# Performance work log

Measured on AMD Instinct MI355X. Metric: run time of the kernel, lower is better.

## Reference

```python
import jax, jax.numpy as jnp
import numpy as np

B, T_DEC, T_ENC = 64, 2048, 512
G_STEPS = 20000          # guided_att_steps
GAMMA = 0.99995          # guided_att_gamma


def setup_inputs() -> dict:
    key = jax.random.key(0)
    k1, k2, k3 = jax.random.split(key, 3)
    alignments = jax.random.uniform(k1, (B, T_DEC, T_ENC), dtype=jnp.float32)
    # ragged lengths in [dim/2, dim] (avoid zero-length -> div by zero)
    input_lengths = jax.random.randint(k2, (B,), T_ENC // 2, T_ENC + 1, dtype=jnp.int32)
    target_lengths = jax.random.randint(k3, (B,), T_DEC // 2, T_DEC + 1, dtype=jnp.int32)
    return {
        "alignments": alignments,
        "input_lengths": input_lengths,
        "target_lengths": target_lengths,
        "global_step": 10000,
    }


def reference(alignments, input_lengths, target_lengths, global_step):
    # matches torch: if self._g_steps < global_step: return 0
    if G_STEPS < global_step:
        return jnp.zeros((), dtype=alignments.dtype)
    g = GAMMA ** global_step  # python float constant
    inv_denom = 1.0 / (2.0 * g * g)

    F = target_lengths.astype(jnp.float32)[:, None, None]   # [B,1,1]
    L = input_lengths.astype(jnp.float32)[:, None, None]    # [B,1,1]
    f = jnp.arange(T_DEC, dtype=jnp.float32)[None, :, None]  # [1,T_dec,1]
    l = jnp.arange(T_ENC, dtype=jnp.float32)[None, None, :]  # [1,1,T_enc]

    # ragged diagonal gaussian mask, zero outside valid [f<F, l<L] region
    w = 1.0 - jnp.exp(-((l / L - f / F) ** 2) * inv_denom)   # [B,T_dec,T_enc]
    valid = (f < F) & (l < L)
    w = jnp.where(valid, w, 0.0)

    per_sample = jnp.sum(w * alignments, axis=(1, 2))        # [B]
    loss = jnp.mean(per_sample / target_lengths.astype(jnp.float32))
    return loss
```

## Files before the change

kernel.cpp:

```cpp
#include <hip/hip_runtime.h>
#include <math.h>


#define BB     64
#define TDEC   2048
#define TENC   512
#define GSTEPS 20000
#define GAMMA  0.99995

#define CHUNKS_PER_B (TDEC * (TENC / 4))
#define TOTAL_CHUNKS (BB * CHUNKS_PER_B)

__global__ void gal_prologue(const int* __restrict__ step_p,
                             float* __restrict__ ws,
                             float* __restrict__ out) {
    int step = step_p[0];
    double g = pow((double)GAMMA, (double)step);
    double inv_denom = 1.0 / (2.0 * g * g);
    ws[0] = (float)inv_denom;
    ((int*)ws)[1] = (GSTEPS < step) ? 0 : 1;
    out[0] = 0.0f;
}

__global__ __launch_bounds__(256) void gal_main(
    const float* __restrict__ align,
    const int* __restrict__ in_len,
    const int* __restrict__ tgt_len,
    const float* __restrict__ ws,
    float* __restrict__ out) {

    const float inv_denom = ws[0];
    const int active = ((const int*)ws)[1];
    if (!active) return;

    __shared__ int   sF[BB];
    __shared__ int   sL[BB];
    __shared__ float sInvF[BB];
    __shared__ float sInvL[BB];
    __shared__ float sScale[BB];
    if (threadIdx.x < BB) {
        int b = threadIdx.x;
        int F = tgt_len[b];
        int L = in_len[b];
        sF[b] = F;
        sL[b] = L;
        float invF = 1.0f / (float)F;
        sInvF[b] = invF;
        sInvL[b] = 1.0f / (float)L;
        sScale[b] = invF * (1.0f / (float)BB);
    }
    __syncthreads();

    float acc = 0.0f;
    const int stride = gridDim.x * blockDim.x;
    for (int i = blockIdx.x * blockDim.x + threadIdx.x; i < TOTAL_CHUNKS; i += stride) {
        const int b   = i >> 18;
        const int rem = i & (CHUNKS_PER_B - 1);
        const int f   = rem >> 7;
        const int l0  = (rem & 127) << 2;

        const int F = sF[b];
        const int L = sL[b];
        if (f >= F || l0 >= L) continue;

        const float4 a = ((const float4*)align)[i];
        const float fd = (float)f * sInvF[b];
        const float invL = sInvL[b];

        float s = 0.0f;
        #pragma unroll
        for (int j = 0; j < 4; ++j) {
            const int l = l0 + j;
            const float d = (float)l * invL - fd;
            const float w = 1.0f - __expf(-(d * d) * inv_denom);
            const float av = (&a.x)[j];
            if (l < L) s += w * av;
        }
        acc += s * sScale[b];
    }

    #pragma unroll
    for (int off = 32; off > 0; off >>= 1) acc += __shfl_down(acc, off, 64);
    __shared__ float swave[4];
    const int lane = threadIdx.x & 63;
    const int wid  = threadIdx.x >> 6;
    if (lane == 0) swave[wid] = acc;
    __syncthreads();
    if (threadIdx.x == 0) {
        float sblk = swave[0] + swave[1] + swave[2] + swave[3];
        atomicAdd(out, sblk);
    }
}

extern "C" void kernel_launch(void* const* d_in, const int* in_sizes, int n_in,
                              void* d_out, int out_size, void* d_ws, size_t ws_size,
                              hipStream_t stream) {
    const float* align   = (const float*)d_in[0];
    const int*   in_len  = (const int*)d_in[1];
    const int*   tgt_len = (const int*)d_in[2];
    const int*   step_p  = (const int*)d_in[3];
    float* out = (float*)d_out;
    float* ws  = (float*)d_ws;

    gal_prologue<<<1, 1, 0, stream>>>(step_p, ws, out);

    const int block = 256;
    const int grid  = 4096;
    gal_main<<<grid, block, 0, stream>>>(align, in_len, tgt_len, ws, out);
}
```

Baseline: 356.2 us.

## Map blocks to per-batch row slabs and skip invalid rows without loading

Replaces the flat grid-stride loop with a fixed mapping: each block owns a 64-row slab of one batch element, and each thread owns a fixed float4 column with per-column normalised positions and masks precomputed. Rows beyond the target length are never visited, which removes the per-chunk index decode, the shared-memory setup and sync, and much of the branch divergence. The exponential now uses exp2 with a prescaled constant, and the weight is applied as acc += a - e*a. Blocks whose slab lies entirely past F exit early, which can leave load imbalance across blocks, and columns past L are still loaded and multiplied by a zero mask.

```diff
diff --git a/kernel.cpp b/kernel.cpp
--- a/kernel.cpp
+++ b/kernel.cpp
@@ -1,5 +1,4 @@
 #include <hip/hip_runtime.h>
-#include <math.h>
 
 
 #define BB     64
@@ -7,17 +6,22 @@
 #define TENC   512
 #define GSTEPS 20000
 #define GAMMA  0.99995
-
-#define CHUNKS_PER_B (TDEC * (TENC / 4))
-#define TOTAL_CHUNKS (BB * CHUNKS_PER_B)
+#define SLABS  32
+#define SLAB_ROWS (TDEC / SLABS)
+#define LOG2E  1.4426950408889634f
 
 __global__ void gal_prologue(const int* __restrict__ step_p,
                              float* __restrict__ ws,
                              float* __restrict__ out) {
     int step = step_p[0];
-    double g = pow((double)GAMMA, (double)step);
-    double inv_denom = 1.0 / (2.0 * g * g);
-    ws[0] = (float)inv_denom;
+    double g = 1.0, base = GAMMA;
+    unsigned e = (step > 0) ? (unsigned)step : 0u;
+    while (e) {
+        if (e & 1u) g *= base;
+        base *= base;
+        e >>= 1;
+    }
+    ws[0] = (float)(1.0 / (2.0 * g * g));
     ((int*)ws)[1] = (GSTEPS < step) ? 0 : 1;
     out[0] = 0.0f;
 }
@@ -29,54 +33,71 @@
     const float* __restrict__ ws,
     float* __restrict__ out) {
 
+    const int b          = blockIdx.x >> 5;
+    const int slab       = blockIdx.x & (SLABS - 1);
+    const int slab_start = slab * SLAB_ROWS;
+
     const float inv_denom = ws[0];
-    const int active = ((const int*)ws)[1];
-    if (!active) return;
+    const int   active    = ((const int*)ws)[1];
 
-    __shared__ int   sF[BB];
-    __shared__ int   sL[BB];
-    __shared__ float sInvF[BB];
-    __shared__ float sInvL[BB];
-    __shared__ float sScale[BB];
-    if (threadIdx.x < BB) {
-        int b = threadIdx.x;
-        int F = tgt_len[b];
-        int L = in_len[b];
-        sF[b] = F;
-        sL[b] = L;
-        float invF = 1.0f / (float)F;
-        sInvF[b] = invF;
-        sInvL[b] = 1.0f / (float)L;
-        sScale[b] = invF * (1.0f / (float)BB);
-    }
-    __syncthreads();
+    const int F = tgt_len[b];
+    const int L = in_len[b];
 
     float acc = 0.0f;
-    const int stride = gridDim.x * blockDim.x;
-    for (int i = blockIdx.x * blockDim.x + threadIdx.x; i < TOTAL_CHUNKS; i += stride) {
-        const int b   = i >> 18;
-        const int rem = i & (CHUNKS_PER_B - 1);
-        const int f   = rem >> 7;
-        const int l0  = (rem & 127) << 2;
 
-        const int F = sF[b];
-        const int L = sL[b];
-        if (f >= F || l0 >= L) continue;
+    const int rows_end = min(slab_start + SLAB_ROWS, F);
+    const int nrows    = rows_end - slab_start;
 
-        const float4 a = ((const float4*)align)[i];
-        const float fd = (float)f * sInvF[b];
-        const float invL = sInvL[b];
+    if (active && nrows > 0) {
+        const int tid = threadIdx.x;
+        const int col = tid & 127;
+        const int r   = tid >> 7;
+        const int l0  = col << 2;
 
-        float s = 0.0f;
+        const float invF = 1.0f / (float)F;
+        const float invL = 1.0f / (float)L;
+        const float c    = -inv_denom * LOG2E;
+
+        float lv[4], cm[4];
         #pragma unroll
         for (int j = 0; j < 4; ++j) {
             const int l = l0 + j;
-            const float d = (float)l * invL - fd;
-            const float w = 1.0f - __expf(-(d * d) * inv_denom);
-            const float av = (&a.x)[j];
-            if (l < L) s += w * av;
+            lv[j] = (float)l * invL;
+            cm[j] = (l < L) ? 1.0f : 0.0f;
         }
-        acc += s * sScale[b];
+
+        const float4* p = (const float4*)(align + ((size_t)b * TDEC + slab_start + r) * TENC) + col;
+        const int nev = nrows & ~1;
+
+        #pragma unroll 4
+        for (int k = 0; k < nev; k += 2) {
+            const float4 a  = *p;
+            const float  fd = (float)(slab_start + k + r) * invF;
+            #pragma unroll
+            for (int j = 0; j < 4; ++j) {
+                const float d   = lv[j] - fd;
+                const float e   = __builtin_amdgcn_exp2f((d * c) * d);
+                const float am  = (&a.x)[j] * cm[j];
+                acc += am;
+                acc  = fmaf(-e, am, acc);
+            }
+            p += 2 * (TENC / 4);
+        }
+
+        if ((nrows & 1) && r == 0) {
+            const float4 a  = *p;
+            const float  fd = (float)(rows_end - 1) * invF;
+            #pragma unroll
+            for (int j = 0; j < 4; ++j) {
+                const float d  = lv[j] - fd;
+                const float e  = __builtin_amdgcn_exp2f((d * c) * d);
+                const float am = (&a.x)[j] * cm[j];
+                acc += am;
+                acc  = fmaf(-e, am, acc);
+            }
+        }
+
+        acc *= invF * (1.0f / (float)BB);
     }
 
     #pragma unroll
@@ -87,8 +108,7 @@
     if (lane == 0) swave[wid] = acc;
     __syncthreads();
     if (threadIdx.x == 0) {
-        float sblk = swave[0] + swave[1] + swave[2] + swave[3];
-        atomicAdd(out, sblk);
+        atomicAdd(out, swave[0] + swave[1] + swave[2] + swave[3]);
     }
 }
 
@@ -104,7 +124,5 @@
 
     gal_prologue<<<1, 1, 0, stream>>>(step_p, ws, out);
 
-    const int block = 256;
-    const int grid  = 4096;
-    gal_main<<<grid, block, 0, stream>>>(align, in_len, tgt_len, ws, out);
+    gal_main<<<BB * SLABS, 256, 0, stream>>>(align, in_len, tgt_len, ws, out);
 }
```

Measured after the change: 347.6 us. -2.4%, faster.
